# Optimization experiments

Measured on AMD Instinct MI355X. Metric: run time of the kernel, lower is better.

Reference implementation:

```python
import jax, jax.numpy as jnp
import numpy as np

N_NODES, N_EDGES, F_IN, F_OUT = 10000, 320000, 256, 256


def setup_inputs() -> dict:
    key = jax.random.key(0)
    k1, k2, k3, k4, k5, k6 = jax.random.split(key, 6)
    feature = jax.random.normal(k1, (N_NODES, F_IN), jnp.float32)
    ew = jax.random.uniform(k2, (N_EDGES,), jnp.float32)          # edge weights
    src = jax.random.randint(k3, (N_EDGES,), 0, N_NODES)
    dst = jax.random.randint(k4, (N_EDGES,), 0, N_NODES)
    # nn.Linear(2*in_feats, out_feats): weight [out, 2*in], bias [out]
    W = jax.random.normal(k5, (F_OUT, 2 * F_IN), jnp.float32) / np.sqrt(2 * F_IN)
    b = jax.random.normal(k6, (F_OUT,), jnp.float32) * 0.01
    return {"feature": feature, "ew": ew, "src": src, "dst": dst, "W": W, "b": b}


def reference(feature, ew, src, dst, W, b):
    n = feature.shape[0]
    # edge_msg2: m[e] = h[src[0]] * h[src[e]] * w[e]   -> [E, F]
    msg = feature[src[0]] * feature[src] * ew[:, None]
    # reduce: segment mean over incoming edges (mailbox mean). The original
    # reduce also computes a segment max concatenated into 'hm', but the apply
    # module only consumes the mean half ('hm_mean', Linear in = 2*in_feats),
    # so the max is dead compute and omitted.
    sums = jax.ops.segment_sum(msg, dst, num_segments=n)
    cnt = jax.ops.segment_sum(jnp.ones((msg.shape[0],), msg.dtype), dst, num_segments=n)
    hm_mean = sums / jnp.maximum(cnt, 1.0)[:, None]
    # NodeApplyModule: relu(Linear(cat(h, hm_mean)))
    x = jnp.concatenate([feature, hm_mean], axis=1)  # [N, 2F]
    return jax.nn.relu(x @ W.T + b)
```

## Files before the change

### kernel.cpp

```cpp
#include <hip/hip_runtime.h>

#define N_NODES 10000
#define N_EDGES 320000
#define F 256
#define K2 512
#define SLOTS 96
#define CSTR 16
#define N_TILE16 625
#define W_BLOCKS 128
#define CNT_BLOCKS 625
#define CONV_BLOCKS 2500
#define PREP_BLOCKS (W_BLOCKS + CNT_BLOCKS + CONV_BLOCKS)
#define SCAT_BLOCKS 1250

typedef __attribute__((ext_vector_type(8))) __bf16 bf16x8;
typedef __attribute__((ext_vector_type(4))) __bf16 bf16x4;
typedef __attribute__((ext_vector_type(4))) float f32x4;
typedef __attribute__((ext_vector_type(2))) float f32x2;
typedef unsigned long long u64;
typedef unsigned int u32;
typedef unsigned short u16;


__global__ __launch_bounds__(256) void prep_conv_kernel(
    const float* __restrict__ feat,
    const float* __restrict__ Wm,
    const int* __restrict__ src,
    __bf16* __restrict__ Wt,
    int* __restrict__ cnt,
    u32* __restrict__ feat8) {
  int b = blockIdx.x;
  int tid = threadIdx.x;
  if (b < W_BLOCKS) {
    int idx = b * 256 + tid;
    int o_ = idx >> 7;
    int k = (idx & 127) * 4;
    float4 w = ((const float4*)Wm)[idx];
    if (k >= F) {
      int s0 = src[0];
      float4 h = ((const float4*)(feat + (size_t)s0 * F))[(k - F) >> 2];
      w.x *= h.x; w.y *= h.y; w.z *= h.z; w.w *= h.w;
    }
    bf16x4 o;
    o[0] = (__bf16)w.x; o[1] = (__bf16)w.y; o[2] = (__bf16)w.z; o[3] = (__bf16)w.w;
    int t = k >> 5, kq = (k & 31) >> 3, e = k & 7;
    size_t offT = (((size_t)t * 4 + kq) * 256 + o_) * 8 + e;
    *(bf16x4*)(Wt + offT) = o;
  } else if (b < W_BLOCKS + CNT_BLOCKS) {
    int idx = (b - W_BLOCKS) * 256 + tid;
    if (idx < N_NODES * CSTR / 4) ((int4*)cnt)[idx] = make_int4(0, 0, 0, 0);
  } else {
    int idx = (b - W_BLOCKS - CNT_BLOCKS) * 256 + tid;
    float4 v = ((const float4*)feat)[idx];
    u32 r8 = 0;
    r8 = __builtin_amdgcn_cvt_pk_fp8_f32(v.x, v.y, r8, false);
    r8 = __builtin_amdgcn_cvt_pk_fp8_f32(v.z, v.w, r8, true);
    feat8[idx] = r8;
  }
}

__global__ __launch_bounds__(256) void scatter_kernel(
    const int* __restrict__ src,
    const int* __restrict__ dst,
    const float* __restrict__ ew,
    int* __restrict__ cnt,
    u32* __restrict__ bucket) {
  int e = blockIdx.x * 256 + threadIdx.x;
  if (e >= N_EDGES) return;
  int d = dst[e];
  u32 wb = (__float_as_uint(ew[e]) + 0x8000u) & 0xFFFF0000u;
  int p = atomicAdd(&cnt[d * CSTR], 1);
  if (p < SLOTS) bucket[(size_t)d * SLOTS + p] = wb | (u32)src[e];
}

__global__ __launch_bounds__(256) void node_agg_kernel(
    const u32* __restrict__ feat8,
    const u32* __restrict__ bucket,
    const int* __restrict__ cnt,
    __bf16* __restrict__ aggb) {
  int node = (blockIdx.x * 256 + threadIdx.x) >> 6;
  int lane = threadIdx.x & 63;
  if (node >= N_NODES) return;
  int c = cnt[node * CSTR];
  int cc = min(c, SLOTS);
  const u32* bk = bucket + (size_t)node * SLOTS;
  const uint2* frow = (const uint2*)feat8;
  const int half = lane >> 5;
  const int slot = lane & 31;

  float acc[8];
#pragma unroll
  for (int e = 0; e < 8; ++e) acc[e] = 0.f;

  for (int i = 0; i < cc; i += 16) {
    u32 p[8];
    uint2 v[8];
#pragma unroll
    for (int j = 0; j < 8; ++j) {
      int e = i + half + 2 * j;
      p[j] = bk[min(e, cc - 1)];
    }
#pragma unroll
    for (int j = 0; j < 8; ++j)
      v[j] = frow[(size_t)(p[j] & 0xFFFFu) * 32 + slot];
#pragma unroll
    for (int j = 0; j < 8; ++j) {
      int e = i + half + 2 * j;
      float w = (e < cc) ? __uint_as_float(p[j] & 0xFFFF0000u) : 0.f;
      f32x2 f01 = __builtin_amdgcn_cvt_pk_f32_fp8(v[j].x, false);
      f32x2 f23 = __builtin_amdgcn_cvt_pk_f32_fp8(v[j].x, true);
      f32x2 f45 = __builtin_amdgcn_cvt_pk_f32_fp8(v[j].y, false);
      f32x2 f67 = __builtin_amdgcn_cvt_pk_f32_fp8(v[j].y, true);
      acc[0] += f01[0] * w; acc[1] += f01[1] * w;
      acc[2] += f23[0] * w; acc[3] += f23[1] * w;
      acc[4] += f45[0] * w; acc[5] += f45[1] * w;
      acc[6] += f67[0] * w; acc[7] += f67[1] * w;
    }
  }

#pragma unroll
  for (int e = 0; e < 8; ++e) acc[e] += __shfl_xor(acc[e], 32, 64);

  if (half == 0) {
    float ic = 1.0f / (float)max(c, 1);
    bf16x8 o;
#pragma unroll
    for (int e = 0; e < 8; ++e) o[e] = (__bf16)(acc[e] * ic);
    *(bf16x8*)(aggb + (size_t)node * F + slot * 8) = o;
  }
}

__global__ __launch_bounds__(512) void mfma_gemm_kernel(
    const float* __restrict__ feat,
    const __bf16* __restrict__ aggb,
    const __bf16* __restrict__ Wt,
    const float* __restrict__ bias,
    float* __restrict__ out) {
  __shared__ float part[4 * 64 * 17];

  const int tid = threadIdx.x;
  const int wave = tid >> 6;
  const int lane = tid & 63;
  const int kh = wave >> 2;
  const int cw = wave & 3;
  const int r15 = lane & 15;
  const int kq = lane >> 4;
  const int col0 = cw * 64;
  const int m0 = blockIdx.x * 16;

  f32x4 acc[4];
#pragma unroll
  for (int cs = 0; cs < 4; ++cs) acc[cs] = (f32x4){0.f, 0.f, 0.f, 0.f};

  if (kh == 0) {
    const float* arow = feat + (size_t)(m0 + r15) * F;
#pragma unroll
    for (int t = 0; t < 8; ++t) {
      float4 lo = *(const float4*)(arow + t * 32 + kq * 8);
      float4 hi = *(const float4*)(arow + t * 32 + kq * 8 + 4);
      bf16x8 a;
      a[0] = (__bf16)lo.x; a[1] = (__bf16)lo.y; a[2] = (__bf16)lo.z; a[3] = (__bf16)lo.w;
      a[4] = (__bf16)hi.x; a[5] = (__bf16)hi.y; a[6] = (__bf16)hi.z; a[7] = (__bf16)hi.w;
#pragma unroll
      for (int cs = 0; cs < 4; ++cs) {
        bf16x8 bb = *(const bf16x8*)(Wt + (((size_t)t * 4 + kq) * 256 + col0 + cs * 16 + r15) * 8);
        acc[cs] = __builtin_amdgcn_mfma_f32_16x16x32_bf16(a, bb, acc[cs], 0, 0, 0);
      }
    }
  } else {
    const __bf16* arow = aggb + (size_t)(m0 + r15) * F;
#pragma unroll
    for (int t2 = 0; t2 < 8; ++t2) {
      bf16x8 a = *(const bf16x8*)(arow + t2 * 32 + kq * 8);
#pragma unroll
      for (int cs = 0; cs < 4; ++cs) {
        bf16x8 bb = *(const bf16x8*)(Wt + (((size_t)(t2 + 8) * 4 + kq) * 256 + col0 + cs * 16 + r15) * 8);
        acc[cs] = __builtin_amdgcn_mfma_f32_16x16x32_bf16(a, bb, acc[cs], 0, 0, 0);
      }
    }
    float* dstp = &part[(cw * 64 + lane) * 17];
#pragma unroll
    for (int cs = 0; cs < 4; ++cs)
#pragma unroll
      for (int r = 0; r < 4; ++r) dstp[cs * 4 + r] = acc[cs][r];
  }
  __syncthreads();

  if (kh == 0) {
    const float* srcp = &part[(cw * 64 + lane) * 17];
    const int rbase = kq * 4;
#pragma unroll
    for (int cs = 0; cs < 4; ++cs) {
      int col = col0 + cs * 16 + r15;
      float bv = bias[col];
#pragma unroll
      for (int r = 0; r < 4; ++r) {
        int orow = m0 + rbase + r;
        float v = acc[cs][r] + srcp[cs * 4 + r] + bv;
        out[(size_t)orow * F + col] = fmaxf(v, 0.0f);
      }
    }
  }
}

extern "C" void kernel_launch(void* const* d_in, const int* in_sizes, int n_in,
                              void* d_out, int out_size, void* d_ws, size_t ws_size,
                              hipStream_t stream) {
  const float* feat = (const float*)d_in[0];
  const float* ew   = (const float*)d_in[1];
  const int*   src  = (const int*)d_in[2];
  const int*   dst  = (const int*)d_in[3];
  const float* Wm   = (const float*)d_in[4];
  const float* bias = (const float*)d_in[5];
  float* out = (float*)d_out;

  u32*    bucket = (u32*)d_ws;
  __bf16* aggb   = (__bf16*)(bucket + (size_t)N_NODES * SLOTS);
  __bf16* Wt     = aggb + (size_t)N_NODES * F;
  u32*    feat8  = (u32*)(Wt + (size_t)F * K2);
  int*    cnt    = (int*)(feat8 + (size_t)N_NODES * F / 4);

  prep_conv_kernel<<<PREP_BLOCKS, 256, 0, stream>>>(feat, Wm, src, Wt, cnt, feat8);
  scatter_kernel<<<SCAT_BLOCKS, 256, 0, stream>>>(src, dst, ew, cnt, bucket);
  node_agg_kernel<<<(N_NODES * 64 + 255) / 256, 256, 0, stream>>>(feat8, bucket, cnt, aggb);
  mfma_gemm_kernel<<<N_TILE16, 512, 0, stream>>>(feat, aggb, Wt, bias, out);
}
```

Before: 57.68 us.

## Merge scatter into prep kernel, pre-convert features to bf16, drop split-K GEMM

Splits count zeroing into its own small kernel so the edge scatter can run inside the same launch as weight and feature conversion. The conversion stage now also writes a bf16 copy of the features. The GEMM reads that copy instead of converting fp32 on the fly, and each wave covers the full K range with no LDS split-K reduction or block sync. GEMM blocks shrink to 256 threads with twice as many of them. The cost is one extra small launch plus an extra 5 MB bf16 feature write and read.

```diff
diff --git a/kernel.cpp b/kernel.cpp
--- a/kernel.cpp
+++ b/kernel.cpp
@@ -6,12 +6,12 @@
 #define K2 512
 #define SLOTS 96
 #define CSTR 16
-#define N_TILE16 625
 #define W_BLOCKS 128
-#define CNT_BLOCKS 625
 #define CONV_BLOCKS 2500
-#define PREP_BLOCKS (W_BLOCKS + CNT_BLOCKS + CONV_BLOCKS)
 #define SCAT_BLOCKS 1250
+#define MAIN_BLOCKS (W_BLOCKS + CONV_BLOCKS + SCAT_BLOCKS)
+#define ZERO_BLOCKS 160
+#define GEMM_BLOCKS 1250
 
 typedef __attribute__((ext_vector_type(8))) __bf16 bf16x8;
 typedef __attribute__((ext_vector_type(4))) __bf16 bf16x4;
@@ -22,13 +22,22 @@
 typedef unsigned short u16;
 
 
-__global__ __launch_bounds__(256) void prep_conv_kernel(
+__global__ __launch_bounds__(256) void zero_kernel(int* __restrict__ cnt) {
+  int idx = blockIdx.x * 256 + threadIdx.x;
+  if (idx < N_NODES * CSTR / 4) ((int4*)cnt)[idx] = make_int4(0, 0, 0, 0);
+}
+
+__global__ __launch_bounds__(256) void main_kernel(
     const float* __restrict__ feat,
     const float* __restrict__ Wm,
     const int* __restrict__ src,
+    const int* __restrict__ dst,
+    const float* __restrict__ ew,
     __bf16* __restrict__ Wt,
+    __bf16* __restrict__ featb,
+    u32* __restrict__ feat8,
     int* __restrict__ cnt,
-    u32* __restrict__ feat8) {
+    u32* __restrict__ bucket) {
   int b = blockIdx.x;
   int tid = threadIdx.x;
   if (b < W_BLOCKS) {
@@ -46,31 +55,24 @@
     int t = k >> 5, kq = (k & 31) >> 3, e = k & 7;
     size_t offT = (((size_t)t * 4 + kq) * 256 + o_) * 8 + e;
     *(bf16x4*)(Wt + offT) = o;
-  } else if (b < W_BLOCKS + CNT_BLOCKS) {
+  } else if (b < W_BLOCKS + CONV_BLOCKS) {
     int idx = (b - W_BLOCKS) * 256 + tid;
-    if (idx < N_NODES * CSTR / 4) ((int4*)cnt)[idx] = make_int4(0, 0, 0, 0);
-  } else {
-    int idx = (b - W_BLOCKS - CNT_BLOCKS) * 256 + tid;
     float4 v = ((const float4*)feat)[idx];
+    bf16x4 o;
+    o[0] = (__bf16)v.x; o[1] = (__bf16)v.y; o[2] = (__bf16)v.z; o[3] = (__bf16)v.w;
+    *(bf16x4*)(featb + (size_t)idx * 4) = o;
     u32 r8 = 0;
     r8 = __builtin_amdgcn_cvt_pk_fp8_f32(v.x, v.y, r8, false);
     r8 = __builtin_amdgcn_cvt_pk_fp8_f32(v.z, v.w, r8, true);
     feat8[idx] = r8;
-  }
-}
-
-__global__ __launch_bounds__(256) void scatter_kernel(
-    const int* __restrict__ src,
-    const int* __restrict__ dst,
-    const float* __restrict__ ew,
-    int* __restrict__ cnt,
-    u32* __restrict__ bucket) {
-  int e = blockIdx.x * 256 + threadIdx.x;
-  if (e >= N_EDGES) return;
-  int d = dst[e];
-  u32 wb = (__float_as_uint(ew[e]) + 0x8000u) & 0xFFFF0000u;
-  int p = atomicAdd(&cnt[d * CSTR], 1);
-  if (p < SLOTS) bucket[(size_t)d * SLOTS + p] = wb | (u32)src[e];
+  } else {
+    int e = (b - W_BLOCKS - CONV_BLOCKS) * 256 + tid;
+    if (e >= N_EDGES) return;
+    int d = dst[e];
+    u32 wb = (__float_as_uint(ew[e]) + 0x8000u) & 0xFFFF0000u;
+    int p = atomicAdd(&cnt[d * CSTR], 1);
+    if (p < SLOTS) bucket[(size_t)d * SLOTS + p] = wb | (u32)src[e];
+  }
 }
 
 __global__ __launch_bounds__(256) void node_agg_kernel(
@@ -130,75 +132,50 @@
   }
 }
 
-__global__ __launch_bounds__(512) void mfma_gemm_kernel(
-    const float* __restrict__ feat,
+__global__ __launch_bounds__(256, 8) void mfma_gemm_kernel(
+    const __bf16* __restrict__ featb,
     const __bf16* __restrict__ aggb,
     const __bf16* __restrict__ Wt,
     const float* __restrict__ bias,
     float* __restrict__ out) {
-  __shared__ float part[4 * 64 * 17];
-
   const int tid = threadIdx.x;
   const int wave = tid >> 6;
   const int lane = tid & 63;
-  const int kh = wave >> 2;
-  const int cw = wave & 3;
   const int r15 = lane & 15;
   const int kq = lane >> 4;
-  const int col0 = cw * 64;
-  const int m0 = blockIdx.x * 16;
-
-  f32x4 acc[4];
-#pragma unroll
-  for (int cs = 0; cs < 4; ++cs) acc[cs] = (f32x4){0.f, 0.f, 0.f, 0.f};
-
-  if (kh == 0) {
-    const float* arow = feat + (size_t)(m0 + r15) * F;
-#pragma unroll
-    for (int t = 0; t < 8; ++t) {
-      float4 lo = *(const float4*)(arow + t * 32 + kq * 8);
-      float4 hi = *(const float4*)(arow + t * 32 + kq * 8 + 4);
-      bf16x8 a;
-      a[0] = (__bf16)lo.x; a[1] = (__bf16)lo.y; a[2] = (__bf16)lo.z; a[3] = (__bf16)lo.w;
-      a[4] = (__bf16)hi.x; a[5] = (__bf16)hi.y; a[6] = (__bf16)hi.z; a[7] = (__bf16)hi.w;
-#pragma unroll
-      for (int cs = 0; cs < 4; ++cs) {
-        bf16x8 bb = *(const bf16x8*)(Wt + (((size_t)t * 4 + kq) * 256 + col0 + cs * 16 + r15) * 8);
-        acc[cs] = __builtin_amdgcn_mfma_f32_16x16x32_bf16(a, bb, acc[cs], 0, 0, 0);
-      }
-    }
-  } else {
-    const __bf16* arow = aggb + (size_t)(m0 + r15) * F;
-#pragma unroll
-    for (int t2 = 0; t2 < 8; ++t2) {
-      bf16x8 a = *(const bf16x8*)(arow + t2 * 32 + kq * 8);
-#pragma unroll
-      for (int cs = 0; cs < 4; ++cs) {
-        bf16x8 bb = *(const bf16x8*)(Wt + (((size_t)(t2 + 8) * 4 + kq) * 256 + col0 + cs * 16 + r15) * 8);
-        acc[cs] = __builtin_amdgcn_mfma_f32_16x16x32_bf16(a, bb, acc[cs], 0, 0, 0);
-      }
-    }
-    float* dstp = &part[(cw * 64 + lane) * 17];
-#pragma unroll
-    for (int cs = 0; cs < 4; ++cs)
-#pragma unroll
-      for (int r = 0; r < 4; ++r) dstp[cs * 4 + r] = acc[cs][r];
-  }
-  __syncthreads();
-
-  if (kh == 0) {
-    const float* srcp = &part[(cw * 64 + lane) * 17];
-    const int rbase = kq * 4;
-#pragma unroll
-    for (int cs = 0; cs < 4; ++cs) {
-      int col = col0 + cs * 16 + r15;
-      float bv = bias[col];
-#pragma unroll
-      for (int r = 0; r < 4; ++r) {
-        int orow = m0 + rbase + r;
-        float v = acc[cs][r] + srcp[cs * 4 + r] + bv;
-        out[(size_t)orow * F + col] = fmaxf(v, 0.0f);
-      }
+  const int mt = blockIdx.x >> 1;
+  const int ch = blockIdx.x & 1;
+  const int col0 = ch * 128 + wave * 32;
+  const int m0 = mt * 16;
+
+  const __bf16* frow = featb + (size_t)(m0 + r15) * F;
+  const __bf16* arow = aggb + (size_t)(m0 + r15) * F;
+
+  f32x4 acc[2];
+  acc[0] = (f32x4){0.f, 0.f, 0.f, 0.f};
+  acc[1] = (f32x4){0.f, 0.f, 0.f, 0.f};
+
+#pragma unroll
+  for (int t = 0; t < 16; ++t) {
+    bf16x8 a;
+    if (t < 8) a = *(const bf16x8*)(frow + t * 32 + kq * 8);
+    else       a = *(const bf16x8*)(arow + (t - 8) * 32 + kq * 8);
+#pragma unroll
+    for (int cs = 0; cs < 2; ++cs) {
+      bf16x8 bb = *(const bf16x8*)(Wt + (((size_t)t * 4 + kq) * 256 + col0 + cs * 16 + r15) * 8);
+      acc[cs] = __builtin_amdgcn_mfma_f32_16x16x32_bf16(a, bb, acc[cs], 0, 0, 0);
+    }
+  }
+
+  const int rbase = kq * 4;
+#pragma unroll
+  for (int cs = 0; cs < 2; ++cs) {
+    int col = col0 + cs * 16 + r15;
+    float bv = bias[col];
+#pragma unroll
+    for (int r = 0; r < 4; ++r) {
+      int orow = m0 + rbase + r;
+      out[(size_t)orow * F + col] = fmaxf(acc[cs][r] + bv, 0.0f);
     }
   }
 }
@@ -215,13 +192,15 @@
   float* out = (float*)d_out;
 
   u32*    bucket = (u32*)d_ws;
-  __bf16* aggb   = (__bf16*)(bucket + (size_t)N_NODES * SLOTS);
+  __bf16* featb  = (__bf16*)(bucket + (size_t)N_NODES * SLOTS);
+  __bf16* aggb   = featb + (size_t)N_NODES * F;
   __bf16* Wt     = aggb + (size_t)N_NODES * F;
   u32*    feat8  = (u32*)(Wt + (size_t)F * K2);
   int*    cnt    = (int*)(feat8 + (size_t)N_NODES * F / 4);
 
-  prep_conv_kernel<<<PREP_BLOCKS, 256, 0, stream>>>(feat, Wm, src, Wt, cnt, feat8);
-  scatter_kernel<<<SCAT_BLOCKS, 256, 0, stream>>>(src, dst, ew, cnt, bucket);
+  zero_kernel<<<ZERO_BLOCKS, 256, 0, stream>>>(cnt);
+  main_kernel<<<MAIN_BLOCKS, 256, 0, stream>>>(feat, Wm, src, dst, ew,
+                                               Wt, featb, feat8, cnt, bucket);
   node_agg_kernel<<<(N_NODES * 64 + 255) / 256, 256, 0, stream>>>(feat8, bucket, cnt, aggb);
-  mfma_gemm_kernel<<<N_TILE16, 512, 0, stream>>>(feat, aggb, Wt, bias, out);
-}
+  mfma_gemm_kernel<<<GEMM_BLOCKS, 256, 0, stream>>>(featb, aggb, Wt, bias, out);
+}
```

Result: slower. 60.69 us (+5.2%).

## Overlap feature-half GEMM with edge scatter and split per-node counters by parity

Applied to the files above, without the earlier changes.

The feature-half GEMM (feature @ W[:, :F]^T + bias) moves into the scatter kernel, running as every third block interleaved with scatter blocks and writing partial output to global memory. The final kernel now only does the aggregate-half GEMM and adds it to the stored partial with relu, so the LDS cross-wave reduction goes away. Scatter atomics are spread over two counters per node by edge parity, each with 48 half-slots, to reduce atomic contention on hot nodes. In exchange the output is read and written twice, and per-parity slot capacity can overflow sooner.

```diff
diff --git a/kernel.cpp b/kernel.cpp
--- a/kernel.cpp
+++ b/kernel.cpp
@@ -4,14 +4,15 @@
 #define N_EDGES 320000
 #define F 256
 #define K2 512
+#define HSLOT 48
 #define SLOTS 96
 #define CSTR 16
-#define N_TILE16 625
 #define W_BLOCKS 128
-#define CNT_BLOCKS 625
+#define CNT_BLOCKS 313
 #define CONV_BLOCKS 2500
 #define PREP_BLOCKS (W_BLOCKS + CNT_BLOCKS + CONV_BLOCKS)
-#define SCAT_BLOCKS 1250
+#define K2_BLOCKS 1875
+#define N_TILE16 625
 
 typedef __attribute__((ext_vector_type(8))) __bf16 bf16x8;
 typedef __attribute__((ext_vector_type(4))) __bf16 bf16x4;
@@ -48,7 +49,7 @@
     *(bf16x4*)(Wt + offT) = o;
   } else if (b < W_BLOCKS + CNT_BLOCKS) {
     int idx = (b - W_BLOCKS) * 256 + tid;
-    if (idx < N_NODES * CSTR / 4) ((int4*)cnt)[idx] = make_int4(0, 0, 0, 0);
+    if (idx < 2 * N_NODES * CSTR / 4) ((int4*)cnt)[idx] = make_int4(0, 0, 0, 0);
   } else {
     int idx = (b - W_BLOCKS - CNT_BLOCKS) * 256 + tid;
     float4 v = ((const float4*)feat)[idx];
@@ -59,18 +60,68 @@
   }
 }
 
-__global__ __launch_bounds__(256) void scatter_kernel(
+__global__ __launch_bounds__(256) void scatter_gemmA_kernel(
+    const float* __restrict__ feat,
     const int* __restrict__ src,
     const int* __restrict__ dst,
     const float* __restrict__ ew,
     int* __restrict__ cnt,
-    u32* __restrict__ bucket) {
-  int e = blockIdx.x * 256 + threadIdx.x;
-  if (e >= N_EDGES) return;
-  int d = dst[e];
-  u32 wb = (__float_as_uint(ew[e]) + 0x8000u) & 0xFFFF0000u;
-  int p = atomicAdd(&cnt[d * CSTR], 1);
-  if (p < SLOTS) bucket[(size_t)d * SLOTS + p] = wb | (u32)src[e];
+    u32* __restrict__ bucket,
+    const __bf16* __restrict__ Wt,
+    const float* __restrict__ bias,
+    float* __restrict__ out) {
+  int b = blockIdx.x;
+  int tid = threadIdx.x;
+  int r3 = b % 3;
+  if (r3 != 2) {
+    int sid = (b / 3) * 2 + r3;
+    int e = sid * 256 + tid;
+    if (e >= N_EDGES) return;
+    int d = dst[e];
+    int par = e & 1;
+    u32 wb = (__float_as_uint(ew[e]) + 0x8000u) & 0xFFFF0000u;
+    int p = atomicAdd(&cnt[(d * 2 + par) * CSTR], 1);
+    if (p < HSLOT) bucket[(size_t)d * SLOTS + par * HSLOT + p] = wb | (u32)src[e];
+  } else {
+    int mt = b / 3;
+    const int wave = tid >> 6;
+    const int lane = tid & 63;
+    const int r15 = lane & 15;
+    const int kq = lane >> 4;
+    const int col0 = wave * 64;
+    const int m0 = mt * 16;
+    const float* arow = feat + (size_t)(m0 + r15) * F;
+
+    f32x4 acc[4];
+#pragma unroll
+    for (int cs = 0; cs < 4; ++cs) acc[cs] = (f32x4){0.f, 0.f, 0.f, 0.f};
+
+#pragma unroll
+    for (int t = 0; t < 8; ++t) {
+      float4 lo = *(const float4*)(arow + t * 32 + kq * 8);
+      float4 hi = *(const float4*)(arow + t * 32 + kq * 8 + 4);
+      bf16x8 a;
+      a[0] = (__bf16)lo.x; a[1] = (__bf16)lo.y; a[2] = (__bf16)lo.z; a[3] = (__bf16)lo.w;
+      a[4] = (__bf16)hi.x; a[5] = (__bf16)hi.y; a[6] = (__bf16)hi.z; a[7] = (__bf16)hi.w;
+#pragma unroll
+      for (int cs = 0; cs < 4; ++cs) {
+        bf16x8 bb = *(const bf16x8*)(Wt + (((size_t)t * 4 + kq) * 256 + col0 + cs * 16 + r15) * 8);
+        acc[cs] = __builtin_amdgcn_mfma_f32_16x16x32_bf16(a, bb, acc[cs], 0, 0, 0);
+      }
+    }
+
+    const int rbase = kq * 4;
+#pragma unroll
+    for (int cs = 0; cs < 4; ++cs) {
+      int col = col0 + cs * 16 + r15;
+      float bv = bias[col];
+#pragma unroll
+      for (int r = 0; r < 4; ++r) {
+        int orow = m0 + rbase + r;
+        out[(size_t)orow * F + col] = acc[cs][r] + bv;
+      }
+    }
+  }
 }
 
 __global__ __launch_bounds__(256) void node_agg_kernel(
@@ -81,8 +132,12 @@
   int node = (blockIdx.x * 256 + threadIdx.x) >> 6;
   int lane = threadIdx.x & 63;
   if (node >= N_NODES) return;
-  int c = cnt[node * CSTR];
-  int cc = min(c, SLOTS);
+  int c0 = cnt[(node * 2) * CSTR];
+  int c1 = cnt[(node * 2 + 1) * CSTR];
+  int cc0 = min(c0, HSLOT);
+  int cc1 = min(c1, HSLOT);
+  int cc = cc0 + cc1;
+  int c = c0 + c1;
   const u32* bk = bucket + (size_t)node * SLOTS;
   const uint2* frow = (const uint2*)feat8;
   const int half = lane >> 5;
@@ -98,7 +153,9 @@
 #pragma unroll
     for (int j = 0; j < 8; ++j) {
       int e = i + half + 2 * j;
-      p[j] = bk[min(e, cc - 1)];
+      int ec = min(e, cc - 1);
+      int si = (ec < cc0) ? ec : (ec - cc0 + HSLOT);
+      p[j] = bk[si];
     }
 #pragma unroll
     for (int j = 0; j < 8; ++j)
@@ -130,75 +187,43 @@
   }
 }
 
-__global__ __launch_bounds__(512) void mfma_gemm_kernel(
-    const float* __restrict__ feat,
+__global__ __launch_bounds__(256) void gemmB_kernel(
     const __bf16* __restrict__ aggb,
     const __bf16* __restrict__ Wt,
-    const float* __restrict__ bias,
     float* __restrict__ out) {
-  __shared__ float part[4 * 64 * 17];
-
   const int tid = threadIdx.x;
   const int wave = tid >> 6;
   const int lane = tid & 63;
-  const int kh = wave >> 2;
-  const int cw = wave & 3;
   const int r15 = lane & 15;
   const int kq = lane >> 4;
-  const int col0 = cw * 64;
+  const int col0 = wave * 64;
   const int m0 = blockIdx.x * 16;
 
+  const __bf16* arow = aggb + (size_t)(m0 + r15) * F;
+
   f32x4 acc[4];
 #pragma unroll
   for (int cs = 0; cs < 4; ++cs) acc[cs] = (f32x4){0.f, 0.f, 0.f, 0.f};
 
-  if (kh == 0) {
-    const float* arow = feat + (size_t)(m0 + r15) * F;
-#pragma unroll
-    for (int t = 0; t < 8; ++t) {
-      float4 lo = *(const float4*)(arow + t * 32 + kq * 8);
-      float4 hi = *(const float4*)(arow + t * 32 + kq * 8 + 4);
-      bf16x8 a;
-      a[0] = (__bf16)lo.x; a[1] = (__bf16)lo.y; a[2] = (__bf16)lo.z; a[3] = (__bf16)lo.w;
-      a[4] = (__bf16)hi.x; a[5] = (__bf16)hi.y; a[6] = (__bf16)hi.z; a[7] = (__bf16)hi.w;
-#pragma unroll
-      for (int cs = 0; cs < 4; ++cs) {
-        bf16x8 bb = *(const bf16x8*)(Wt + (((size_t)t * 4 + kq) * 256 + col0 + cs * 16 + r15) * 8);
-        acc[cs] = __builtin_amdgcn_mfma_f32_16x16x32_bf16(a, bb, acc[cs], 0, 0, 0);
-      }
-    }
-  } else {
-    const __bf16* arow = aggb + (size_t)(m0 + r15) * F;
-#pragma unroll
-    for (int t2 = 0; t2 < 8; ++t2) {
-      bf16x8 a = *(const bf16x8*)(arow + t2 * 32 + kq * 8);
-#pragma unroll
-      for (int cs = 0; cs < 4; ++cs) {
-        bf16x8 bb = *(const bf16x8*)(Wt + (((size_t)(t2 + 8) * 4 + kq) * 256 + col0 + cs * 16 + r15) * 8);
-        acc[cs] = __builtin_amdgcn_mfma_f32_16x16x32_bf16(a, bb, acc[cs], 0, 0, 0);
-      }
-    }
-    float* dstp = &part[(cw * 64 + lane) * 17];
-#pragma unroll
-    for (int cs = 0; cs < 4; ++cs)
-#pragma unroll
-      for (int r = 0; r < 4; ++r) dstp[cs * 4 + r] = acc[cs][r];
-  }
-  __syncthreads();
-
-  if (kh == 0) {
-    const float* srcp = &part[(cw * 64 + lane) * 17];
-    const int rbase = kq * 4;
+#pragma unroll
+  for (int t2 = 0; t2 < 8; ++t2) {
+    bf16x8 a = *(const bf16x8*)(arow + t2 * 32 + kq * 8);
 #pragma unroll
     for (int cs = 0; cs < 4; ++cs) {
-      int col = col0 + cs * 16 + r15;
-      float bv = bias[col];
-#pragma unroll
-      for (int r = 0; r < 4; ++r) {
-        int orow = m0 + rbase + r;
-        float v = acc[cs][r] + srcp[cs * 4 + r] + bv;
-        out[(size_t)orow * F + col] = fmaxf(v, 0.0f);
-      }
+      bf16x8 bb = *(const bf16x8*)(Wt + (((size_t)(t2 + 8) * 4 + kq) * 256 + col0 + cs * 16 + r15) * 8);
+      acc[cs] = __builtin_amdgcn_mfma_f32_16x16x32_bf16(a, bb, acc[cs], 0, 0, 0);
+    }
+  }
+
+  const int rbase = kq * 4;
+#pragma unroll
+  for (int cs = 0; cs < 4; ++cs) {
+    int col = col0 + cs * 16 + r15;
+#pragma unroll
+    for (int r = 0; r < 4; ++r) {
+      int orow = m0 + rbase + r;
+      size_t oi = (size_t)orow * F + col;
+      out[oi] = fmaxf(out[oi] + acc[cs][r], 0.0f);
     }
   }
 }
@@ -221,7 +246,8 @@
   int*    cnt    = (int*)(feat8 + (size_t)N_NODES * F / 4);
 
   prep_conv_kernel<<<PREP_BLOCKS, 256, 0, stream>>>(feat, Wm, src, Wt, cnt, feat8);
-  scatter_kernel<<<SCAT_BLOCKS, 256, 0, stream>>>(src, dst, ew, cnt, bucket);
+  scatter_gemmA_kernel<<<K2_BLOCKS, 256, 0, stream>>>(feat, src, dst, ew,
+                                                      cnt, bucket, Wt, bias, out);
   node_agg_kernel<<<(N_NODES * 64 + 255) / 256, 256, 0, stream>>>(feat8, bucket, cnt, aggb);
-  mfma_gemm_kernel<<<N_TILE16, 512, 0, stream>>>(feat, aggb, Wt, bias, out);
-}
+  gemmB_kernel<<<N_TILE16, 256, 0, stream>>>(aggb, Wt, out);
+}
```

New measurement: 55.30 us. 1.04x faster.
